# Kernel tuning notes

Hardware: AMD Instinct MI355X
Metric: run time of the kernel (lower is better)

The kernel has to match this reference:

```python
import jax, jax.numpy as jnp
import numpy as np

IN_CH, OUT_CH, HEAD, QK_DIM, V_DIM = 256, 256, 8, 512, 512


def setup_inputs() -> dict:
    key = jax.random.key(0)
    ks = jax.random.split(key, 5)
    B, H, W = 16, 32, 32
    x = jax.random.normal(ks[0], (B, IN_CH, H, W), dtype=jnp.float32)
    # 1x1 conv weights stored as [out_ch, in_ch]
    qkv_out = 2 * QK_DIM + V_DIM
    qkv_w = jax.random.normal(ks[1], (qkv_out, IN_CH), dtype=jnp.float32) * (IN_CH ** -0.5)
    qkv_b = jax.random.normal(ks[2], (qkv_out,), dtype=jnp.float32) * 0.02
    proj_w = jax.random.normal(ks[3], (OUT_CH, V_DIM), dtype=jnp.float32) * (V_DIM ** -0.5)
    proj_b = jax.random.normal(ks[4], (OUT_CH,), dtype=jnp.float32) * 0.02
    return {"x": x, "qkv_w": qkv_w, "qkv_b": qkv_b, "proj_w": proj_w, "proj_b": proj_b}


def reference(x, qkv_w, qkv_b, proj_w, proj_b):
    B, C, H, W = x.shape
    N = H * W
    dh = QK_DIM // HEAD
    dv = V_DIM // HEAD
    scale = dh ** -0.5
    # 1x1 conv == channel GEMM
    qkv = jnp.einsum('bchw,oc->bohw', x, qkv_w) + qkv_b[None, :, None, None]
    q, k, v = jnp.split(qkv, [QK_DIM, 2 * QK_DIM], axis=1)
    # [B, ch, H, W] -> [B, head, N, head_dim]
    def to_heads(t, d):
        return t.reshape(B, HEAD, d, N).transpose(0, 1, 3, 2)
    q = to_heads(q, dh)
    k = to_heads(k, dh)
    v = to_heads(v, dv)
    mask = jnp.tril(jnp.ones((N, N), dtype=bool))  # [N, N]
    scores = jnp.einsum('bhnd,bhmd->bhnm', q, k) * scale
    scores = jnp.where(mask, scores, -jnp.inf)
    attn = jax.nn.softmax(scores, axis=-1)
    attn = jnp.where(mask, attn, 0.0)
    out = jnp.einsum('bhnm,bhmd->bhnd', attn, v)  # [B, head, N, dv]
    out = out.transpose(0, 1, 3, 2).reshape(B, V_DIM, H, W)
    out = jnp.einsum('bvhw,ov->bohw', out, proj_w) + proj_b[None, :, None, None]
    return out
```

## Files before the change

kernel.cpp:

```cpp
#include <hip/hip_runtime.h>
#include <math.h>

static constexpr int Bsz = 16;
static constexpr int Np  = 1024;
static constexpr int Cin = 256;

typedef __attribute__((ext_vector_type(8))) short short8;
typedef __attribute__((ext_vector_type(4))) float f4;

__device__ __forceinline__ unsigned short f2b(float f) {
    union { float fp; unsigned int u; } v; v.fp = f;
    unsigned int r = v.u + 0x7fffu + ((v.u >> 16) & 1u);
    return (unsigned short)(r >> 16);
}

__global__ __launch_bounds__(256)
void cast_x(const float* __restrict__ x, ushort* __restrict__ xb)
{
    __shared__ ushort T[64][72];
    const int t = threadIdx.x;
    const int n0 = blockIdx.x * 64, c0 = blockIdx.y * 64, b = blockIdx.z;

    {
        const int c_l = t >> 2, ns = (t & 3) * 16;
        const float* src = &x[((b * Cin + c0 + c_l) << 10) + n0 + ns];
#pragma unroll
        for (int i = 0; i < 4; ++i) {
            const float4 v = *(const float4*)(src + 4 * i);
            T[ns + 4 * i + 0][c_l] = f2b(v.x);
            T[ns + 4 * i + 1][c_l] = f2b(v.y);
            T[ns + 4 * i + 2][c_l] = f2b(v.z);
            T[ns + 4 * i + 3][c_l] = f2b(v.w);
        }
    }
    __syncthreads();
    {
        const int n_l = t >> 2, cs = (t & 3) * 16;
        ushort* dst = &xb[((b << 10) + n0 + n_l) * Cin + c0 + cs];
        *(uint4*)dst       = *(const uint4*)&T[n_l][cs];
        *(uint4*)(dst + 8) = *(const uint4*)&T[n_l][cs + 8];
    }
}

__global__ __launch_bounds__(256)
void cast_w(const float* __restrict__ qw, const float* __restrict__ pw,
            ushort* __restrict__ qwb, ushort* __restrict__ pwb)
{
    const int i = blockIdx.x * 256 + threadIdx.x;
    const int nq4 = (1536 * 256) / 4;
    const float* src; ushort* dst; int j;
    if (i < nq4) { src = qw; dst = qwb; j = i; }
    else         { src = pw; dst = pwb; j = i - nq4; }
    const float4 v = *(const float4*)(src + 4 * j);
    ushort4 u; u.x = f2b(v.x); u.y = f2b(v.y); u.z = f2b(v.z); u.w = f2b(v.w);
    *(ushort4*)(dst + 4 * j) = u;
}

__global__ __launch_bounds__(256)
void qkv_gemm(const ushort* __restrict__ xb, const ushort* __restrict__ wb,
              const float* __restrict__ bias,
              ushort* __restrict__ qb, ushort* __restrict__ kb, ushort* __restrict__ vb)
{
    __shared__ ushort lds[17408];
    ushort* As = lds;
    ushort* Bs = lds + 5120;

    const int t = threadIdx.x;
    const int w = t >> 6, lane = t & 63, quad = lane >> 4, ln = lane & 15;
    const int n0 = blockIdx.x * 128;
    const int o0 = blockIdx.y * 128;
    const int b  = blockIdx.z;
    const int ow = (w & 1) * 64, nw = (w >> 1) * 64;
    const bool vpath = (o0 >= 1024);

    f4 acc[4][4];
#pragma unroll
    for (int i = 0; i < 4; ++i)
#pragma unroll
        for (int j = 0; j < 4; ++j) acc[i][j] = (f4){0.f, 0.f, 0.f, 0.f};

    const int r = t >> 1, hh = (t & 1) * 16;
    for (int k0 = 0; k0 < Cin; k0 += 32) {
        __syncthreads();
        {
            const ushort* sa = &wb[(o0 + r) * Cin + k0 + hh];
            *(uint4*)&As[r * 40 + hh]     = *(const uint4*)sa;
            *(uint4*)&As[r * 40 + hh + 8] = *(const uint4*)(sa + 8);
            const ushort* sb = &xb[((b << 10) + n0 + r) * Cin + k0 + hh];
            *(uint4*)&Bs[r * 40 + hh]     = *(const uint4*)sb;
            *(uint4*)&Bs[r * 40 + hh + 8] = *(const uint4*)(sb + 8);
        }
        __syncthreads();
        short8 af[4], bf[4];
#pragma unroll
        for (int ot = 0; ot < 4; ++ot)
            af[ot] = *(const short8*)&As[(ow + ot * 16 + ln) * 40 + quad * 8];
#pragma unroll
        for (int nt = 0; nt < 4; ++nt)
            bf[nt] = *(const short8*)&Bs[(nw + nt * 16 + ln) * 40 + quad * 8];
        if (!vpath) {
#pragma unroll
            for (int ot = 0; ot < 4; ++ot)
#pragma unroll
                for (int nt = 0; nt < 4; ++nt)
                    acc[ot][nt] = __builtin_amdgcn_mfma_f32_16x16x32_bf16(
                        af[ot], bf[nt], acc[ot][nt], 0, 0, 0);
        } else {
#pragma unroll
            for (int nt = 0; nt < 4; ++nt)
#pragma unroll
                for (int ot = 0; ot < 4; ++ot)
                    acc[nt][ot] = __builtin_amdgcn_mfma_f32_16x16x32_bf16(
                        bf[nt], af[ot], acc[nt][ot], 0, 0, 0);
        }
    }

    __syncthreads();
    if (!vpath) {
        ushort* Ct = lds;
        const float sc = (o0 < 512) ? 0.125f : 1.0f;
#pragma unroll
        for (int ot = 0; ot < 4; ++ot) {
            float bs[4];
#pragma unroll
            for (int rg = 0; rg < 4; ++rg)
                bs[rg] = bias[o0 + ow + ot * 16 + quad * 4 + rg];
#pragma unroll
            for (int nt = 0; nt < 4; ++nt) {
                ushort4 u;
                u.x = f2b((acc[ot][nt][0] + bs[0]) * sc);
                u.y = f2b((acc[ot][nt][1] + bs[1]) * sc);
                u.z = f2b((acc[ot][nt][2] + bs[2]) * sc);
                u.w = f2b((acc[ot][nt][3] + bs[3]) * sc);
                *(ushort4*)&Ct[(nw + nt * 16 + ln) * 136 + ow + ot * 16 + quad * 4] = u;
            }
        }
        __syncthreads();
        ushort* dst; int obase;
        if (o0 < 512) { dst = qb; obase = o0; }
        else          { dst = kb; obase = o0 - 512; }
        const int rn = t >> 1, hf = t & 1;
        const int bh = b * 8 + (obase >> 6) + hf;
        ushort* drow = &dst[(bh * Np + n0 + rn) << 6];
        const ushort* srow = &Ct[rn * 136 + hf * 64];
#pragma unroll
        for (int s = 0; s < 8; ++s)
            *(uint4*)(drow + s * 8) = *(const uint4*)(srow + s * 8);
    } else {
        ushort* Ct = lds;
#pragma unroll
        for (int ot = 0; ot < 4; ++ot) {
            const float bo = bias[o0 + ow + ot * 16 + ln];
#pragma unroll
            for (int nt = 0; nt < 4; ++nt) {
                ushort4 u;
                u.x = f2b(acc[nt][ot][0] + bo);
                u.y = f2b(acc[nt][ot][1] + bo);
                u.z = f2b(acc[nt][ot][2] + bo);
                u.w = f2b(acc[nt][ot][3] + bo);
                *(ushort4*)&Ct[(ow + ot * 16 + ln) * 136 + nw + nt * 16 + quad * 4] = u;
            }
        }
        __syncthreads();
        const int o_l = t >> 1, nh = (t & 1) * 64;
        const int bh = b * 8 + ((o0 - 1024) >> 6) + (o_l >> 6);
        ushort* drow = &vb[((size_t)bh << 16) + ((o_l & 63) << 10) + n0 + nh];
        const ushort* srow = &Ct[o_l * 136 + nh];
#pragma unroll
        for (int s = 0; s < 8; ++s)
            *(uint4*)(drow + s * 8) = *(const uint4*)(srow + s * 8);
    }
}

__global__ __launch_bounds__(256, 4)
void attn(const ushort* __restrict__ qb, const ushort* __restrict__ kb,
          const ushort* __restrict__ vt, ushort* __restrict__ ob)
{
    __shared__ ushort Qs[64 * 72];
    __shared__ ushort Ks[64 * 72];
    __shared__ ushort Vt[64 * 72];
    __shared__ ushort Ps[64 * 72];

    const int t    = threadIdx.x;
    const int w    = t >> 6;
    const int lane = t & 63;
    const int quad = lane >> 4;
    const int ln   = lane & 15;
    const int bh   = blockIdx.x & 127;
    const int qt   = 15 - (blockIdx.x >> 7);
    const int q0   = qt * 64;

    {
        const int r = t & 63, seg = t >> 6;
        const ushort* src = &qb[((bh * Np + q0 + r) << 6) + seg * 16];
        *(uint4*)&Qs[r * 72 + seg * 16]     = *(const uint4*)src;
        *(uint4*)&Qs[r * 72 + seg * 16 + 8] = *(const uint4*)(src + 8);
    }
    __syncthreads();

    const short8 qa0 = *(const short8*)&Qs[(w * 16 + ln) * 72 + quad * 8];
    const short8 qa1 = *(const short8*)&Qs[(w * 16 + ln) * 72 + 32 + quad * 8];

    f4 o_[4];
#pragma unroll
    for (int nt = 0; nt < 4; ++nt) o_[nt] = (f4){0.f, 0.f, 0.f, 0.f};
    float mrun = -INFINITY, lrun = 0.f;

    for (int kt = 0; kt <= qt; ++kt) {
        __syncthreads();
        {
            const int r = t & 63, seg = t >> 6;
            const ushort* sk = &kb[((bh * Np + kt * 64 + r) << 6) + seg * 16];
            *(uint4*)&Ks[r * 72 + seg * 16]     = *(const uint4*)sk;
            *(uint4*)&Ks[r * 72 + seg * 16 + 8] = *(const uint4*)(sk + 8);
            const int dd = t >> 2, c = (t & 3) * 16;
            const ushort* sv = &vt[((size_t)bh << 16) + (dd << 10) + kt * 64 + c];
            *(uint4*)&Vt[dd * 72 + c]     = *(const uint4*)sv;
            *(uint4*)&Vt[dd * 72 + c + 8] = *(const uint4*)(sv + 8);
        }
        __syncthreads();

        const bool diag = (kt == qt);

        f4 st[4];
#pragma unroll
        for (int mt = 0; mt < 4; ++mt) st[mt] = (f4){0.f, 0.f, 0.f, 0.f};
#pragma unroll
        for (int mt = 0; mt < 4; ++mt) {
            if (diag && mt > w) continue;
            const short8 ka0 = *(const short8*)&Ks[(mt * 16 + ln) * 72 + quad * 8];
            const short8 ka1 = *(const short8*)&Ks[(mt * 16 + ln) * 72 + 32 + quad * 8];
            st[mt] = __builtin_amdgcn_mfma_f32_16x16x32_bf16(ka0, qa0, st[mt], 0, 0, 0);
            st[mt] = __builtin_amdgcn_mfma_f32_16x16x32_bf16(ka1, qa1, st[mt], 0, 0, 0);
        }

        if (diag) {
            const int qrow = w * 16 + ln;
#pragma unroll
            for (int mt = 0; mt < 4; ++mt)
#pragma unroll
                for (int rg = 0; rg < 4; ++rg)
                    if (mt * 16 + quad * 4 + rg > qrow) st[mt][rg] = -INFINITY;
        }

        float mx = -INFINITY;
#pragma unroll
        for (int mt = 0; mt < 4; ++mt)
#pragma unroll
            for (int rg = 0; rg < 4; ++rg) mx = fmaxf(mx, st[mt][rg]);
        mx = fmaxf(mx, __shfl_xor(mx, 16));
        mx = fmaxf(mx, __shfl_xor(mx, 32));

        const float mn = fmaxf(mrun, mx);
        const float al = __expf(mrun - mn);
        mrun = mn;

        float rs = 0.f;
        const int prow = (w * 16 + ln) * 72;
#pragma unroll
        for (int mt = 0; mt < 4; ++mt) {
            float p0 = __expf(st[mt][0] - mn), p1 = __expf(st[mt][1] - mn);
            float p2 = __expf(st[mt][2] - mn), p3 = __expf(st[mt][3] - mn);
            rs += (p0 + p1) + (p2 + p3);
            ushort4 u; u.x = f2b(p0); u.y = f2b(p1); u.z = f2b(p2); u.w = f2b(p3);
            *(ushort4*)&Ps[prow + mt * 16 + quad * 4] = u;
        }
        rs += __shfl_xor(rs, 16);
        rs += __shfl_xor(rs, 32);
        lrun = lrun * al + rs;

        float alr[4];
#pragma unroll
        for (int rg = 0; rg < 4; ++rg) alr[rg] = __shfl(al, quad * 4 + rg);
#pragma unroll
        for (int nt = 0; nt < 4; ++nt)
#pragma unroll
            for (int rg = 0; rg < 4; ++rg) o_[nt][rg] *= alr[rg];

#pragma unroll
        for (int ks = 0; ks < 2; ++ks) {
            if (diag && w * 16 + 15 < ks * 32) continue;
            const short8 pa = *(const short8*)&Ps[prow + ks * 32 + quad * 8];
#pragma unroll
            for (int nt = 0; nt < 4; ++nt) {
                const short8 vf = *(const short8*)&Vt[(nt * 16 + ln) * 72 + ks * 32 + quad * 8];
                o_[nt] = __builtin_amdgcn_mfma_f32_16x16x32_bf16(pa, vf, o_[nt], 0, 0, 0);
            }
        }
    }

    const float linv = 1.0f / lrun;
    float lr[4];
#pragma unroll
    for (int rg = 0; rg < 4; ++rg) lr[rg] = __shfl(linv, quad * 4 + rg);
#pragma unroll
    for (int rg = 0; rg < 4; ++rg) {
        const int rr = q0 + w * 16 + quad * 4 + rg;
#pragma unroll
        for (int nt = 0; nt < 4; ++nt)
            ob[((bh * Np + rr) << 6) + nt * 16 + ln] = f2b(o_[nt][rg] * lr[rg]);
    }
}

__global__ __launch_bounds__(256)
void proj_gemm(const ushort* __restrict__ obuf, const ushort* __restrict__ pwb,
               const float* __restrict__ bias, float* __restrict__ out)
{
    __shared__ ushort As[128 * 40];
    __shared__ ushort Bs[128 * 40];

    const int t = threadIdx.x;
    const int w = t >> 6, lane = t & 63, quad = lane >> 4, ln = lane & 15;
    const int n0 = blockIdx.x * 128;
    const int o0 = blockIdx.y * 128;
    const int b  = blockIdx.z;
    const int ow = (w & 1) * 64, nw = (w >> 1) * 64;

    f4 acc[4][4];
#pragma unroll
    for (int i = 0; i < 4; ++i)
#pragma unroll
        for (int j = 0; j < 4; ++j) acc[i][j] = (f4){0.f, 0.f, 0.f, 0.f};

    const int r = t >> 1, hh = (t & 1) * 16;
    for (int k0 = 0; k0 < 512; k0 += 32) {
        __syncthreads();
        {
            const ushort* sa = &pwb[(o0 + r) * 512 + k0 + hh];
            *(uint4*)&As[r * 40 + hh]     = *(const uint4*)sa;
            *(uint4*)&As[r * 40 + hh + 8] = *(const uint4*)(sa + 8);
            const int head = k0 >> 6, kc = k0 & 63;
            const ushort* sb = &obuf[(((b * 8 + head) * Np + n0 + r) << 6) + kc + hh];
            *(uint4*)&Bs[r * 40 + hh]     = *(const uint4*)sb;
            *(uint4*)&Bs[r * 40 + hh + 8] = *(const uint4*)(sb + 8);
        }
        __syncthreads();
        short8 af[4], bf[4];
#pragma unroll
        for (int ot = 0; ot < 4; ++ot)
            af[ot] = *(const short8*)&As[(ow + ot * 16 + ln) * 40 + quad * 8];
#pragma unroll
        for (int nt = 0; nt < 4; ++nt)
            bf[nt] = *(const short8*)&Bs[(nw + nt * 16 + ln) * 40 + quad * 8];
#pragma unroll
        for (int ot = 0; ot < 4; ++ot)
#pragma unroll
            for (int nt = 0; nt < 4; ++nt)
                acc[ot][nt] = __builtin_amdgcn_mfma_f32_16x16x32_bf16(
                    af[ot], bf[nt], acc[ot][nt], 0, 0, 0);
    }

#pragma unroll
    for (int ot = 0; ot < 4; ++ot) {
        float bs[4];
#pragma unroll
        for (int rg = 0; rg < 4; ++rg)
            bs[rg] = bias[o0 + ow + ot * 16 + quad * 4 + rg];
#pragma unroll
        for (int rg = 0; rg < 4; ++rg) {
            const int oo = o0 + ow + ot * 16 + quad * 4 + rg;
            float* drow = &out[((b << 8) + oo) << 10];
#pragma unroll
            for (int nt = 0; nt < 4; ++nt)
                drow[n0 + nw + nt * 16 + ln] = acc[ot][nt][rg] + bs[rg];
        }
    }
}

extern "C" void kernel_launch(void* const* d_in, const int* in_sizes, int n_in,
                              void* d_out, int out_size, void* d_ws, size_t ws_size,
                              hipStream_t stream)
{
    const float* x   = (const float*)d_in[0];
    const float* qw  = (const float*)d_in[1];
    const float* qbb = (const float*)d_in[2];
    const float* pw  = (const float*)d_in[3];
    const float* pb  = (const float*)d_in[4];
    float* out = (float*)d_out;

    const size_t per = (size_t)Bsz * 8 * Np * 64;
    ushort* qbuf = (ushort*)d_ws;
    ushort* kbuf = qbuf + per;
    ushort* vbuf = kbuf + per;
    ushort* obuf = vbuf + per;
    ushort* xb   = obuf + per;
    ushort* qwb  = xb + (size_t)Bsz * Np * Cin;
    ushort* pwb  = qwb + 1536 * Cin;

    cast_x<<<dim3(16, 4, Bsz), 256, 0, stream>>>(x, xb);
    cast_w<<<dim3(512), 256, 0, stream>>>(qw, pw, qwb, pwb);
    qkv_gemm<<<dim3(8, 12, Bsz), 256, 0, stream>>>(xb, qwb, qbb, qbuf, kbuf, vbuf);
    attn<<<dim3(128 * 16), 256, 0, stream>>>(qbuf, kbuf, vbuf, obuf);
    proj_gemm<<<dim3(8, 2, Bsz), 256, 0, stream>>>(obuf, pwb, pb, out);
}
```

Measured before the change: 180.7 us.

## Merge cast kernels, widen GEMM K-tiles, shrink proj tile, use exp2 softmax

Merges the x and weight cast kernels into one launch, dropping one kernel launch. Both GEMMs now stage K=64 per LDS step instead of 32, which halves the number of barriers. The projection GEMM uses 64-row output tiles so that twice as many blocks fill the device. The Q pre-scale now folds in log2(e), so the attention softmax can use the hardware exp2 directly instead of __expf. The cost is more LDS per block, which may reduce occupancy.

Result: faster. 164.8 us (-8.8%).

```diff
diff --git a/kernel.cpp b/kernel.cpp
--- a/kernel.cpp
+++ b/kernel.cpp
@@ -7,6 +7,18 @@
 
 typedef __attribute__((ext_vector_type(8))) short short8;
 typedef __attribute__((ext_vector_type(4))) float f4;
+
+#if defined(__has_builtin)
+#if __has_builtin(__builtin_amdgcn_exp2f)
+#define EXP2(x) __builtin_amdgcn_exp2f(x)
+#else
+#define EXP2(x) exp2f(x)
+#endif
+#else
+#define EXP2(x) exp2f(x)
+#endif
+
+#define QSCALE 0.18033688011112f
 
 __device__ __forceinline__ unsigned short f2b(float f) {
     union { float fp; unsigned int u; } v; v.fp = f;
@@ -15,45 +27,47 @@
 }
 
 __global__ __launch_bounds__(256)
-void cast_x(const float* __restrict__ x, ushort* __restrict__ xb)
+void cast_xw(const float* __restrict__ x, const float* __restrict__ qw,
+             const float* __restrict__ pw, ushort* __restrict__ xb,
+             ushort* __restrict__ qwb, ushort* __restrict__ pwb)
 {
-    __shared__ ushort T[64][72];
     const int t = threadIdx.x;
-    const int n0 = blockIdx.x * 64, c0 = blockIdx.y * 64, b = blockIdx.z;
-
-    {
-        const int c_l = t >> 2, ns = (t & 3) * 16;
-        const float* src = &x[((b * Cin + c0 + c_l) << 10) + n0 + ns];
-#pragma unroll
-        for (int i = 0; i < 4; ++i) {
-            const float4 v = *(const float4*)(src + 4 * i);
-            T[ns + 4 * i + 0][c_l] = f2b(v.x);
-            T[ns + 4 * i + 1][c_l] = f2b(v.y);
-            T[ns + 4 * i + 2][c_l] = f2b(v.z);
-            T[ns + 4 * i + 3][c_l] = f2b(v.w);
-        }
-    }
-    __syncthreads();
-    {
-        const int n_l = t >> 2, cs = (t & 3) * 16;
-        ushort* dst = &xb[((b << 10) + n0 + n_l) * Cin + c0 + cs];
-        *(uint4*)dst       = *(const uint4*)&T[n_l][cs];
-        *(uint4*)(dst + 8) = *(const uint4*)&T[n_l][cs + 8];
-    }
-}
-
-__global__ __launch_bounds__(256)
-void cast_w(const float* __restrict__ qw, const float* __restrict__ pw,
-            ushort* __restrict__ qwb, ushort* __restrict__ pwb)
-{
-    const int i = blockIdx.x * 256 + threadIdx.x;
-    const int nq4 = (1536 * 256) / 4;
-    const float* src; ushort* dst; int j;
-    if (i < nq4) { src = qw; dst = qwb; j = i; }
-    else         { src = pw; dst = pwb; j = i - nq4; }
-    const float4 v = *(const float4*)(src + 4 * j);
-    ushort4 u; u.x = f2b(v.x); u.y = f2b(v.y); u.z = f2b(v.z); u.w = f2b(v.w);
-    *(ushort4*)(dst + 4 * j) = u;
+    if (blockIdx.y < 4) {
+        __shared__ ushort T[64][72];
+        const int n0 = blockIdx.x * 64, c0 = blockIdx.y * 64, b = blockIdx.z;
+        {
+            const int c_l = t >> 2, ns = (t & 3) * 16;
+            const float* src = &x[((b * Cin + c0 + c_l) << 10) + n0 + ns];
+#pragma unroll
+            for (int i = 0; i < 4; ++i) {
+                const float4 v = *(const float4*)(src + 4 * i);
+                T[ns + 4 * i + 0][c_l] = f2b(v.x);
+                T[ns + 4 * i + 1][c_l] = f2b(v.y);
+                T[ns + 4 * i + 2][c_l] = f2b(v.z);
+                T[ns + 4 * i + 3][c_l] = f2b(v.w);
+            }
+        }
+        __syncthreads();
+        {
+            const int n_l = t >> 2, cs = (t & 3) * 16;
+            ushort* dst = &xb[((b << 10) + n0 + n_l) * Cin + c0 + cs];
+            *(uint4*)dst       = *(const uint4*)&T[n_l][cs];
+            *(uint4*)(dst + 8) = *(const uint4*)&T[n_l][cs + 8];
+        }
+    } else {
+        const int nq4 = (1536 * Cin) / 4;
+        const int base = ((blockIdx.z * 16 + blockIdx.x) * 256 + t) * 2;
+#pragma unroll
+        for (int g = 0; g < 2; ++g) {
+            const int j = base + g;
+            const float* src; ushort* dst; int jj;
+            if (j < nq4) { src = qw; dst = qwb; jj = j; }
+            else         { src = pw; dst = pwb; jj = j - nq4; }
+            const float4 v = *(const float4*)(src + 4 * jj);
+            ushort4 u; u.x = f2b(v.x); u.y = f2b(v.y); u.z = f2b(v.z); u.w = f2b(v.w);
+            *(ushort4*)(dst + 4 * jj) = u;
+        }
+    }
 }
 
 __global__ __launch_bounds__(256)
@@ -61,9 +75,9 @@
               const float* __restrict__ bias,
               ushort* __restrict__ qb, ushort* __restrict__ kb, ushort* __restrict__ vb)
 {
-    __shared__ ushort lds[17408];
+    __shared__ ushort lds[18432];
     ushort* As = lds;
-    ushort* Bs = lds + 5120;
+    ushort* Bs = lds + 9216;
 
     const int t = threadIdx.x;
     const int w = t >> 6, lane = t & 63, quad = lane >> 4, ln = lane & 15;
@@ -79,46 +93,51 @@
 #pragma unroll
         for (int j = 0; j < 4; ++j) acc[i][j] = (f4){0.f, 0.f, 0.f, 0.f};
 
-    const int r = t >> 1, hh = (t & 1) * 16;
-    for (int k0 = 0; k0 < Cin; k0 += 32) {
-        __syncthreads();
-        {
-            const ushort* sa = &wb[(o0 + r) * Cin + k0 + hh];
-            *(uint4*)&As[r * 40 + hh]     = *(const uint4*)sa;
-            *(uint4*)&As[r * 40 + hh + 8] = *(const uint4*)(sa + 8);
-            const ushort* sb = &xb[((b << 10) + n0 + r) * Cin + k0 + hh];
-            *(uint4*)&Bs[r * 40 + hh]     = *(const uint4*)sb;
-            *(uint4*)&Bs[r * 40 + hh + 8] = *(const uint4*)(sb + 8);
-        }
-        __syncthreads();
-        short8 af[4], bf[4];
-#pragma unroll
-        for (int ot = 0; ot < 4; ++ot)
-            af[ot] = *(const short8*)&As[(ow + ot * 16 + ln) * 40 + quad * 8];
-#pragma unroll
-        for (int nt = 0; nt < 4; ++nt)
-            bf[nt] = *(const short8*)&Bs[(nw + nt * 16 + ln) * 40 + quad * 8];
-        if (!vpath) {
+    const int rr = t >> 2, cc = (t & 3) * 16;
+    for (int k0 = 0; k0 < Cin; k0 += 64) {
+        __syncthreads();
+#pragma unroll
+        for (int p = 0; p < 2; ++p) {
+            const int row = rr + p * 64;
+            const ushort* sa = &wb[(o0 + row) * Cin + k0 + cc];
+            *(uint4*)&As[row * 72 + cc]     = *(const uint4*)sa;
+            *(uint4*)&As[row * 72 + cc + 8] = *(const uint4*)(sa + 8);
+            const ushort* sb = &xb[((b << 10) + n0 + row) * Cin + k0 + cc];
+            *(uint4*)&Bs[row * 72 + cc]     = *(const uint4*)sb;
+            *(uint4*)&Bs[row * 72 + cc + 8] = *(const uint4*)(sb + 8);
+        }
+        __syncthreads();
+#pragma unroll
+        for (int sub = 0; sub < 2; ++sub) {
+            short8 af[4], bf[4];
 #pragma unroll
             for (int ot = 0; ot < 4; ++ot)
+                af[ot] = *(const short8*)&As[(ow + ot * 16 + ln) * 72 + sub * 32 + quad * 8];
+#pragma unroll
+            for (int nt = 0; nt < 4; ++nt)
+                bf[nt] = *(const short8*)&Bs[(nw + nt * 16 + ln) * 72 + sub * 32 + quad * 8];
+            if (!vpath) {
+#pragma unroll
+                for (int ot = 0; ot < 4; ++ot)
+#pragma unroll
+                    for (int nt = 0; nt < 4; ++nt)
+                        acc[ot][nt] = __builtin_amdgcn_mfma_f32_16x16x32_bf16(
+                            af[ot], bf[nt], acc[ot][nt], 0, 0, 0);
+            } else {
 #pragma unroll
                 for (int nt = 0; nt < 4; ++nt)
-                    acc[ot][nt] = __builtin_amdgcn_mfma_f32_16x16x32_bf16(
-                        af[ot], bf[nt], acc[ot][nt], 0, 0, 0);
-        } else {
-#pragma unroll
-            for (int nt = 0; nt < 4; ++nt)
-#pragma unroll
-                for (int ot = 0; ot < 4; ++ot)
-                    acc[nt][ot] = __builtin_amdgcn_mfma_f32_16x16x32_bf16(
-                        bf[nt], af[ot], acc[nt][ot], 0, 0, 0);
+#pragma unroll
+                    for (int ot = 0; ot < 4; ++ot)
+                        acc[nt][ot] = __builtin_amdgcn_mfma_f32_16x16x32_bf16(
+                            bf[nt], af[ot], acc[nt][ot], 0, 0, 0);
+            }
         }
     }
 
     __syncthreads();
     if (!vpath) {
         ushort* Ct = lds;
-        const float sc = (o0 < 512) ? 0.125f : 1.0f;
+        const float sc = (o0 < 512) ? QSCALE : 1.0f;
 #pragma unroll
         for (int ot = 0; ot < 4; ++ot) {
             float bs[4];
@@ -252,15 +271,15 @@
         mx = fmaxf(mx, __shfl_xor(mx, 32));
 
         const float mn = fmaxf(mrun, mx);
-        const float al = __expf(mrun - mn);
+        const float al = EXP2(mrun - mn);
         mrun = mn;
 
         float rs = 0.f;
         const int prow = (w * 16 + ln) * 72;
 #pragma unroll
         for (int mt = 0; mt < 4; ++mt) {
-            float p0 = __expf(st[mt][0] - mn), p1 = __expf(st[mt][1] - mn);
-            float p2 = __expf(st[mt][2] - mn), p3 = __expf(st[mt][3] - mn);
+            float p0 = EXP2(st[mt][0] - mn), p1 = EXP2(st[mt][1] - mn);
+            float p2 = EXP2(st[mt][2] - mn), p3 = EXP2(st[mt][3] - mn);
             rs += (p0 + p1) + (p2 + p3);
             ushort4 u; u.x = f2b(p0); u.y = f2b(p1); u.z = f2b(p2); u.w = f2b(p3);
             *(ushort4*)&Ps[prow + mt * 16 + quad * 4] = u;
@@ -306,63 +325,67 @@
 void proj_gemm(const ushort* __restrict__ obuf, const ushort* __restrict__ pwb,
                const float* __restrict__ bias, float* __restrict__ out)
 {
-    __shared__ ushort As[128 * 40];
-    __shared__ ushort Bs[128 * 40];
+    __shared__ ushort As[64 * 72];
+    __shared__ ushort Bs[128 * 72];
 
     const int t = threadIdx.x;
     const int w = t >> 6, lane = t & 63, quad = lane >> 4, ln = lane & 15;
     const int n0 = blockIdx.x * 128;
-    const int o0 = blockIdx.y * 128;
+    const int o0 = blockIdx.y * 64;
     const int b  = blockIdx.z;
-    const int ow = (w & 1) * 64, nw = (w >> 1) * 64;
-
-    f4 acc[4][4];
+    const int nw = w * 32;
+
+    f4 acc[4][2];
 #pragma unroll
     for (int i = 0; i < 4; ++i)
 #pragma unroll
-        for (int j = 0; j < 4; ++j) acc[i][j] = (f4){0.f, 0.f, 0.f, 0.f};
-
-    const int r = t >> 1, hh = (t & 1) * 16;
-    for (int k0 = 0; k0 < 512; k0 += 32) {
+        for (int j = 0; j < 2; ++j) acc[i][j] = (f4){0.f, 0.f, 0.f, 0.f};
+
+    const int rr = t >> 2, cc = (t & 3) * 16;
+    for (int k0 = 0; k0 < 512; k0 += 64) {
         __syncthreads();
         {
-            const ushort* sa = &pwb[(o0 + r) * 512 + k0 + hh];
-            *(uint4*)&As[r * 40 + hh]     = *(const uint4*)sa;
-            *(uint4*)&As[r * 40 + hh + 8] = *(const uint4*)(sa + 8);
-            const int head = k0 >> 6, kc = k0 & 63;
-            const ushort* sb = &obuf[(((b * 8 + head) * Np + n0 + r) << 6) + kc + hh];
-            *(uint4*)&Bs[r * 40 + hh]     = *(const uint4*)sb;
-            *(uint4*)&Bs[r * 40 + hh + 8] = *(const uint4*)(sb + 8);
-        }
-        __syncthreads();
-        short8 af[4], bf[4];
-#pragma unroll
-        for (int ot = 0; ot < 4; ++ot)
-            af[ot] = *(const short8*)&As[(ow + ot * 16 + ln) * 40 + quad * 8];
-#pragma unroll
-        for (int nt = 0; nt < 4; ++nt)
-            bf[nt] = *(const short8*)&Bs[(nw + nt * 16 + ln) * 40 + quad * 8];
-#pragma unroll
-        for (int ot = 0; ot < 4; ++ot)
-#pragma unroll
-            for (int nt = 0; nt < 4; ++nt)
-                acc[ot][nt] = __builtin_amdgcn_mfma_f32_16x16x32_bf16(
-                    af[ot], bf[nt], acc[ot][nt], 0, 0, 0);
+            const ushort* sa = &pwb[(o0 + rr) * 512 + k0 + cc];
+            *(uint4*)&As[rr * 72 + cc]     = *(const uint4*)sa;
+            *(uint4*)&As[rr * 72 + cc + 8] = *(const uint4*)(sa + 8);
+            const int head = k0 >> 6;
+#pragma unroll
+            for (int p = 0; p < 2; ++p) {
+                const int row = rr + p * 64;
+                const ushort* sb = &obuf[(((b * 8 + head) * Np + n0 + row) << 6) + cc];
+                *(uint4*)&Bs[row * 72 + cc]     = *(const uint4*)sb;
+                *(uint4*)&Bs[row * 72 + cc + 8] = *(const uint4*)(sb + 8);
+            }
+        }
+        __syncthreads();
+#pragma unroll
+        for (int sub = 0; sub < 2; ++sub) {
+            short8 af[4], bf[2];
+#pragma unroll
+            for (int ot = 0; ot < 4; ++ot)
+                af[ot] = *(const short8*)&As[(ot * 16 + ln) * 72 + sub * 32 + quad * 8];
+#pragma unroll
+            for (int nt = 0; nt < 2; ++nt)
+                bf[nt] = *(const short8*)&Bs[(nw + nt * 16 + ln) * 72 + sub * 32 + quad * 8];
+#pragma unroll
+            for (int ot = 0; ot < 4; ++ot)
+#pragma unroll
+                for (int nt = 0; nt < 2; ++nt)
+                    acc[ot][nt] = __builtin_amdgcn_mfma_f32_16x16x32_bf16(
+                        af[ot], bf[nt], acc[ot][nt], 0, 0, 0);
+        }
     }
 
 #pragma unroll
     for (int ot = 0; ot < 4; ++ot) {
-        float bs[4];
-#pragma unroll
-        for (int rg = 0; rg < 4; ++rg)
-            bs[rg] = bias[o0 + ow + ot * 16 + quad * 4 + rg];
 #pragma unroll
         for (int rg = 0; rg < 4; ++rg) {
-            const int oo = o0 + ow + ot * 16 + quad * 4 + rg;
+            const int oo = o0 + ot * 16 + quad * 4 + rg;
+            const float pb = bias[oo];
             float* drow = &out[((b << 8) + oo) << 10];
 #pragma unroll
-            for (int nt = 0; nt < 4; ++nt)
-                drow[n0 + nw + nt * 16 + ln] = acc[ot][nt][rg] + bs[rg];
+            for (int nt = 0; nt < 2; ++nt)
+                drow[n0 + nw + nt * 16 + ln] = acc[ot][nt][rg] + pb;
         }
     }
 }
@@ -387,9 +410,8 @@
     ushort* qwb  = xb + (size_t)Bsz * Np * Cin;
     ushort* pwb  = qwb + 1536 * Cin;
 
-    cast_x<<<dim3(16, 4, Bsz), 256, 0, stream>>>(x, xb);
-    cast_w<<<dim3(512), 256, 0, stream>>>(qw, pw, qwb, pwb);
+    cast_xw<<<dim3(16, 5, Bsz), 256, 0, stream>>>(x, qw, pw, xb, qwb, pwb);
     qkv_gemm<<<dim3(8, 12, Bsz), 256, 0, stream>>>(xb, qwb, qbb, qbuf, kbuf, vbuf);
     attn<<<dim3(128 * 16), 256, 0, stream>>>(qbuf, kbuf, vbuf, obuf);
-    proj_gemm<<<dim3(8, 2, Bsz), 256, 0, stream>>>(obuf, pwb, pb, out);
-}
+    proj_gemm<<<dim3(8, 4, Bsz), 256, 0, stream>>>(obuf, pwb, pb, out);
+}
```
